# Kernel tuning notes

Hardware: AMD Instinct MI355X
Metric: run time of the kernel (lower is better)

Reference implementation:

```python
import jax, jax.numpy as jnp
import numpy as np

B, T, L = 512, 1024, 48


def setup_inputs() -> dict:
    key = jax.random.key(0)
    k1, k2, k3 = jax.random.split(key, 3)
    # one-hot gold labels [B, T, L]
    labels = jax.random.randint(k1, (B, T), 0, L)
    y_true = jax.nn.one_hot(labels, L, dtype=jnp.float32)
    y_pred = jax.random.normal(k2, (B, T, L), dtype=jnp.float32)
    trans = jax.random.normal(k3, (L, L), dtype=jnp.float32) * 0.1  # crf_trans weight
    return {"y_true": y_true, "y_pred": y_pred, "trans": trans}


def reference(y_true, y_pred, trans):
    # --- log normalization constant via forward algorithm (scan over time) ---
    init = y_pred[:, 0]                       # [B, L] initial alpha
    xs = jnp.moveaxis(y_pred[:, 1:], 1, 0)    # [T-1, B, L] emissions per step

    def step(alpha, emit):
        # alpha[b, i] + trans[i, j] -> logsumexp over i -> add emission j
        nxt = jax.nn.logsumexp(alpha[:, :, None] + trans[None, :, :], axis=1) + emit
        return nxt, None

    alpha_last, _ = jax.lax.scan(step, init, xs)          # [B, L]
    log_norm = jax.nn.logsumexp(alpha_last, axis=1, keepdims=True)  # [B, 1]

    # --- unnormalized path score: emissions + transitions along gold path ---
    point_score = jnp.sum(y_pred * y_true, axis=(1, 2))[:, None]  # [B, 1]
    trans_score = jnp.einsum("btl,lm,btm->b", y_true[:, :-1], trans, y_true[:, 1:])[:, None]

    return log_norm - point_score - trans_score  # [B, 1] negative log-likelihood
```

## Files before the change

### kernel.cpp

```cpp
#include <hip/hip_runtime.h>


constexpr int Bb = 512;
constexpr int Tt = 1024;
constexpr int Ll = 48;
constexpr int PF = 4;

#define LOG2E_F 1.44269504088896340736f
#define LN2_F   0.69314718055994530942f

__device__ __forceinline__ float rl_f(float v, int l) {
    return __uint_as_float(__builtin_amdgcn_readlane(__float_as_uint(v), (unsigned)l));
}
__device__ __forceinline__ float fexp2(float x) {
    return __builtin_amdgcn_exp2f(x);
}
__device__ __forceinline__ float flog2(float x) {
    return __builtin_amdgcn_logf(x);
}

__global__ __launch_bounds__(64)
__attribute__((amdgpu_waves_per_eu(1, 1)))
void crf_fwd_kernel(const float* __restrict__ y_true,
                    const float* __restrict__ y_pred,
                    const float* __restrict__ trans,
                    float* __restrict__ out)
{
    const int lane = threadIdx.x;

    __shared__ float str[Ll * Ll];

    if (blockIdx.x >= Bb) {
        const int b = blockIdx.x - Bb;
        for (int i = lane; i < Ll * Ll; i += 64) str[i] = trans[i];
        __syncthreads();

        const float* __restrict__ yprow = y_pred + (size_t)b * Tt * Ll;
        const float* __restrict__ ytrow = y_true + (size_t)b * Tt * Ll;

        float ps = 0.f, ts = 0.f;
        int labLast = 0;

        for (int t0 = 0; t0 < Tt; t0 += 64) {
            const int t = t0 + lane;
            const float4* row = (const float4*)(ytrow + (size_t)t * Ll);
            int lab = 0;
            #pragma unroll
            for (int k = 0; k < 12; ++k) {
                float4 v = row[k];
                if (v.x > 0.5f) lab = 4 * k + 0;
                if (v.y > 0.5f) lab = 4 * k + 1;
                if (v.z > 0.5f) lab = 4 * k + 2;
                if (v.w > 0.5f) lab = 4 * k + 3;
            }
            ps += yprow[(size_t)t * Ll + lab];
            int labPrev = __shfl_up(lab, 1);
            if (lane == 0) labPrev = labLast;
            if (t > 0) ts += str[labPrev * Ll + lab];
            labLast = __builtin_amdgcn_readlane(lab, 63);
        }

        float acc = ps + ts;
        #pragma unroll
        for (int off = 32; off >= 1; off >>= 1) acc += __shfl_xor(acc, off);
        if (lane == 0) atomicAdd(&out[b], -acc);
        return;
    }

    const int b  = blockIdx.x;
    const int ml = lane < Ll ? lane : (Ll - 1);
    const bool act = lane < Ll;
    for (int i = lane; i < Ll * Ll; i += 64) str[i] = trans[i];
    __syncthreads();

#define MK_E(l) float E##l = fexp2(str[(l) * Ll + ml] * LOG2E_F);
    MK_E(0)  MK_E(1)  MK_E(2)  MK_E(3)  MK_E(4)  MK_E(5)  MK_E(6)  MK_E(7)
    MK_E(8)  MK_E(9)  MK_E(10) MK_E(11) MK_E(12) MK_E(13) MK_E(14) MK_E(15)
    MK_E(16) MK_E(17) MK_E(18) MK_E(19) MK_E(20) MK_E(21) MK_E(22) MK_E(23)
    MK_E(24) MK_E(25) MK_E(26) MK_E(27) MK_E(28) MK_E(29) MK_E(30) MK_E(31)
    MK_E(32) MK_E(33) MK_E(34) MK_E(35) MK_E(36) MK_E(37) MK_E(38) MK_E(39)
    MK_E(40) MK_E(41) MK_E(42) MK_E(43) MK_E(44) MK_E(45) MK_E(46) MK_E(47)
#undef MK_E

    const float* __restrict__ yprow = y_pred + (size_t)b * Tt * Ll;

    float raw0 = yprow[ml];
    float e = fexp2(raw0 * LOG2E_F);
    float S = 0.f;
    float cUse = 0.5f * rl_f(raw0, 0) * LOG2E_F;

#define RLF(l, acc) acc = fmaf(rl_f(e, l), E##l, acc);

#define STEP(raw)                                                        \
    do {                                                                 \
        float cNew = 0.5f * flog2(rl_f(e, 0));                           \
        cNew = fminf(50.f, fmaxf(-50.f, cNew));                          \
        float w = fexp2(fmaf((raw), LOG2E_F, -cUse));                    \
        S += cUse;                                                       \
        cUse = cNew;                                                     \
        float a0 = 0.f, a1 = 0.f, a2 = 0.f, a3 = 0.f;                    \
        float a4 = 0.f, a5 = 0.f, a6 = 0.f, a7 = 0.f;                    \
        RLF(0,  a0) RLF(1,  a1) RLF(2,  a2) RLF(3,  a3)                  \
        RLF(4,  a4) RLF(5,  a5) RLF(6,  a6) RLF(7,  a7)                  \
        RLF(8,  a0) RLF(9,  a1) RLF(10, a2) RLF(11, a3)                  \
        RLF(12, a4) RLF(13, a5) RLF(14, a6) RLF(15, a7)                  \
        RLF(16, a0) RLF(17, a1) RLF(18, a2) RLF(19, a3)                  \
        RLF(20, a4) RLF(21, a5) RLF(22, a6) RLF(23, a7)                  \
        RLF(24, a0) RLF(25, a1) RLF(26, a2) RLF(27, a3)                  \
        RLF(28, a4) RLF(29, a5) RLF(30, a6) RLF(31, a7)                  \
        RLF(32, a0) RLF(33, a1) RLF(34, a2) RLF(35, a3)                  \
        RLF(36, a4) RLF(37, a5) RLF(38, a6) RLF(39, a7)                  \
        RLF(40, a0) RLF(41, a1) RLF(42, a2) RLF(43, a3)                  \
        RLF(44, a4) RLF(45, a5) RLF(46, a6) RLF(47, a7)                  \
        e = (((a0 + a1) + (a2 + a3)) + ((a4 + a5) + (a6 + a7))) * w;     \
    } while (0)

    float pfP[PF];
    #pragma unroll
    for (int j = 0; j < PF; ++j) pfP[j] = yprow[(1 + j) * Ll + ml];

    for (int t0 = 1; t0 <= Tt - PF - 3; t0 += PF) {
        #pragma unroll
        for (int j = 0; j < PF; ++j) {
            float raw = pfP[j];
            int tn = t0 + j + PF;
            tn = tn < Tt ? tn : (Tt - 1);
            pfP[j] = yprow[tn * Ll + ml];
            STEP(raw);
        }
    }
    STEP(pfP[0]);
    STEP(pfP[1]);
    STEP(pfP[2]);
#undef STEP
#undef RLF

    float es = act ? e : 0.f;
    #pragma unroll
    for (int off = 32; off >= 1; off >>= 1) es += __shfl_xor(es, off);

    if (lane == 0)
        atomicAdd(&out[b], LN2_F * (S + flog2(es)));
}

extern "C" void kernel_launch(void* const* d_in, const int* in_sizes, int n_in,
                              void* d_out, int out_size, void* d_ws, size_t ws_size,
                              hipStream_t stream) {
    const float* y_true = (const float*)d_in[0];
    const float* y_pred = (const float*)d_in[1];
    const float* trans  = (const float*)d_in[2];
    float* out = (float*)d_out;

    hipMemsetAsync(d_out, 0, (size_t)out_size * sizeof(float), stream);
    crf_fwd_kernel<<<2 * Bb, 64, 0, stream>>>(y_true, y_pred, trans, out);
}
```

Before: 182.8 us.

## Replace readlane broadcast matvec with DPP row_ror fmac and bpermute row rotation

The per-step 48x48 matvec previously broadcast each alpha lane with v_readlane (SALU-to-VALU round trips) before every fma. It now splits the 48 states into three 16-lane rows, fetches the two other rows with ds_bpermute, and uses v_fmac with DPP row_ror modifiers so each fma reads a rotated neighbour lane directly. The transition exponentials are precomputed in the matching rotated order using a probe of the row_ror lane mapping. This cuts the scalar readlane traffic in exchange for two LDS permutes per step and hand-written inline asm with s_nop hazard padding, which risks subtle correctness issues (lanes 48-63 use the clamped row).

```diff
diff --git a/kernel.cpp b/kernel.cpp
--- a/kernel.cpp
+++ b/kernel.cpp
@@ -12,12 +12,8 @@
 __device__ __forceinline__ float rl_f(float v, int l) {
     return __uint_as_float(__builtin_amdgcn_readlane(__float_as_uint(v), (unsigned)l));
 }
-__device__ __forceinline__ float fexp2(float x) {
-    return __builtin_amdgcn_exp2f(x);
-}
-__device__ __forceinline__ float flog2(float x) {
-    return __builtin_amdgcn_logf(x);
-}
+__device__ __forceinline__ float fexp2(float x) { return __builtin_amdgcn_exp2f(x); }
+__device__ __forceinline__ float flog2(float x) { return __builtin_amdgcn_logf(x); }
 
 __global__ __launch_bounds__(64)
 __attribute__((amdgpu_waves_per_eu(1, 1)))
@@ -70,17 +66,29 @@
     const int b  = blockIdx.x;
     const int ml = lane < Ll ? lane : (Ll - 1);
     const bool act = lane < Ll;
+    const int g = lane >> 4;
+    const int r = lane & 15;
     for (int i = lane; i < Ll * Ll; i += 64) str[i] = trans[i];
     __syncthreads();
 
-#define MK_E(l) float E##l = fexp2(str[(l) * Ll + ml] * LOG2E_F);
-    MK_E(0)  MK_E(1)  MK_E(2)  MK_E(3)  MK_E(4)  MK_E(5)  MK_E(6)  MK_E(7)
-    MK_E(8)  MK_E(9)  MK_E(10) MK_E(11) MK_E(12) MK_E(13) MK_E(14) MK_E(15)
-    MK_E(16) MK_E(17) MK_E(18) MK_E(19) MK_E(20) MK_E(21) MK_E(22) MK_E(23)
-    MK_E(24) MK_E(25) MK_E(26) MK_E(27) MK_E(28) MK_E(29) MK_E(30) MK_E(31)
-    MK_E(32) MK_E(33) MK_E(34) MK_E(35) MK_E(36) MK_E(37) MK_E(38) MK_E(39)
-    MK_E(40) MK_E(41) MK_E(42) MK_E(43) MK_E(44) MK_E(45) MK_E(46) MK_E(47)
-#undef MK_E
+#define PROBE(i) int P##i; \
+    asm volatile("s_nop 1\n\tv_mov_b32 %0, %1 row_ror:" #i : "=v"(P##i) : "v"(lane));
+    PROBE(1)  PROBE(2)  PROBE(3)  PROBE(4)  PROBE(5)  PROBE(6)  PROBE(7)
+    PROBE(8)  PROBE(9)  PROBE(10) PROBE(11) PROBE(12) PROBE(13) PROBE(14) PROBE(15)
+#undef PROBE
+
+#define MK_C(c, i, SR) float C_##c##_##i = \
+    fexp2(str[(16 * ((g + (c)) % 3) + (SR)) * Ll + ml] * LOG2E_F);
+#define MK_CI(i) MK_C(0, i, (P##i & 15)) MK_C(1, i, (P##i & 15)) MK_C(2, i, (P##i & 15))
+    MK_C(0, 0, r) MK_C(1, 0, r) MK_C(2, 0, r)
+    MK_CI(1)  MK_CI(2)  MK_CI(3)  MK_CI(4)  MK_CI(5)
+    MK_CI(6)  MK_CI(7)  MK_CI(8)  MK_CI(9)  MK_CI(10)
+    MK_CI(11) MK_CI(12) MK_CI(13) MK_CI(14) MK_CI(15)
+#undef MK_CI
+#undef MK_C
+
+    int idx1 = 4 * (16 * ((g + 1) % 3) + r);
+    int idx2 = 4 * (16 * ((g + 2) % 3) + r);
 
     const float* __restrict__ yprow = y_pred + (size_t)b * Tt * Ll;
 
@@ -89,10 +97,17 @@
     float S = 0.f;
     float cUse = 0.5f * rl_f(raw0, 0) * LOG2E_F;
 
-#define RLF(l, acc) acc = fmaf(rl_f(e, l), E##l, acc);
+#define FD(c, i, acc) asm volatile("v_fmac_f32 %0, %1, %2 row_ror:" #i \
+        : "+v"(acc) : "v"(ec##c), "v"(C_##c##_##i));
+#define F0(c, acc) asm volatile("v_fmac_f32 %0, %1, %2" \
+        : "+v"(acc) : "v"(ec##c), "v"(C_##c##_0));
 
 #define STEP(raw)                                                        \
     do {                                                                 \
+        int ei = __float_as_uint(e);                                     \
+        float ec0 = e;                                                   \
+        float ec1 = __uint_as_float((unsigned)__builtin_amdgcn_ds_bpermute(idx1, ei)); \
+        float ec2 = __uint_as_float((unsigned)__builtin_amdgcn_ds_bpermute(idx2, ei)); \
         float cNew = 0.5f * flog2(rl_f(e, 0));                           \
         cNew = fminf(50.f, fmaxf(-50.f, cNew));                          \
         float w = fexp2(fmaf((raw), LOG2E_F, -cUse));                    \
@@ -100,18 +115,19 @@
         cUse = cNew;                                                     \
         float a0 = 0.f, a1 = 0.f, a2 = 0.f, a3 = 0.f;                    \
         float a4 = 0.f, a5 = 0.f, a6 = 0.f, a7 = 0.f;                    \
-        RLF(0,  a0) RLF(1,  a1) RLF(2,  a2) RLF(3,  a3)                  \
-        RLF(4,  a4) RLF(5,  a5) RLF(6,  a6) RLF(7,  a7)                  \
-        RLF(8,  a0) RLF(9,  a1) RLF(10, a2) RLF(11, a3)                  \
-        RLF(12, a4) RLF(13, a5) RLF(14, a6) RLF(15, a7)                  \
-        RLF(16, a0) RLF(17, a1) RLF(18, a2) RLF(19, a3)                  \
-        RLF(20, a4) RLF(21, a5) RLF(22, a6) RLF(23, a7)                  \
-        RLF(24, a0) RLF(25, a1) RLF(26, a2) RLF(27, a3)                  \
-        RLF(28, a4) RLF(29, a5) RLF(30, a6) RLF(31, a7)                  \
-        RLF(32, a0) RLF(33, a1) RLF(34, a2) RLF(35, a3)                  \
-        RLF(36, a4) RLF(37, a5) RLF(38, a6) RLF(39, a7)                  \
-        RLF(40, a0) RLF(41, a1) RLF(42, a2) RLF(43, a3)                  \
-        RLF(44, a4) RLF(45, a5) RLF(46, a6) RLF(47, a7)                  \
+        asm volatile("s_nop 1");                                         \
+        F0(0, a0)      FD(0, 1,  a1) FD(0, 2,  a2) FD(0, 3,  a3)         \
+        FD(0, 4,  a4)  FD(0, 5,  a5) FD(0, 6,  a6) FD(0, 7,  a7)         \
+        FD(0, 8,  a0)  FD(0, 9,  a1) FD(0, 10, a2) FD(0, 11, a3)         \
+        FD(0, 12, a4)  FD(0, 13, a5) FD(0, 14, a6) FD(0, 15, a7)         \
+        F0(1, a0)      FD(1, 1,  a1) FD(1, 2,  a2) FD(1, 3,  a3)         \
+        FD(1, 4,  a4)  FD(1, 5,  a5) FD(1, 6,  a6) FD(1, 7,  a7)         \
+        FD(1, 8,  a0)  FD(1, 9,  a1) FD(1, 10, a2) FD(1, 11, a3)         \
+        FD(1, 12, a4)  FD(1, 13, a5) FD(1, 14, a6) FD(1, 15, a7)         \
+        F0(2, a0)      FD(2, 1,  a1) FD(2, 2,  a2) FD(2, 3,  a3)         \
+        FD(2, 4,  a4)  FD(2, 5,  a5) FD(2, 6,  a6) FD(2, 7,  a7)         \
+        FD(2, 8,  a0)  FD(2, 9,  a1) FD(2, 10, a2) FD(2, 11, a3)         \
+        FD(2, 12, a4)  FD(2, 13, a5) FD(2, 14, a6) FD(2, 15, a7)         \
         e = (((a0 + a1) + (a2 + a3)) + ((a4 + a5) + (a6 + a7))) * w;     \
     } while (0)
 
@@ -133,7 +149,8 @@
     STEP(pfP[1]);
     STEP(pfP[2]);
 #undef STEP
-#undef RLF
+#undef FD
+#undef F0
 
     float es = act ? e : 0.f;
     #pragma unroll
```

Measured after the change: 235.4 us. 28.8% more time.

## Batch 16 sequences per wave and compute CRF forward step with bf16 MFMA

Applied to the files above, without the earlier changes.

Replaces the per-sequence readlane/FMA matrix-vector product with a batched matrix product. Each wave now handles 16 sequences, and the exp(trans) times alpha step for all of them runs on bf16 MFMA 16x16x32 instructions. This cuts the forward-pass block count from 512 to 32 and removes the 48 serial readlanes per step. In exchange, alpha is rounded to bf16 at every step, which costs accuracy, and far fewer waves remain to hide the serial latency chain.

```diff
diff --git a/kernel.cpp b/kernel.cpp
--- a/kernel.cpp
+++ b/kernel.cpp
@@ -4,19 +4,27 @@
 constexpr int Bb = 512;
 constexpr int Tt = 1024;
 constexpr int Ll = 48;
-constexpr int PF = 4;
+constexpr int NC = 16;
+constexpr int NSB = Bb / NC;
 
 #define LOG2E_F 1.44269504088896340736f
 #define LN2_F   0.69314718055994530942f
 
-__device__ __forceinline__ float rl_f(float v, int l) {
-    return __uint_as_float(__builtin_amdgcn_readlane(__float_as_uint(v), (unsigned)l));
+typedef short bf16x8 __attribute__((ext_vector_type(8)));
+typedef float f32x4  __attribute__((ext_vector_type(4)));
+typedef unsigned int u32x4 __attribute__((ext_vector_type(4)));
+
+__device__ __forceinline__ float fexp2(float x) { return __builtin_amdgcn_exp2f(x); }
+__device__ __forceinline__ float flog2(float x) { return __builtin_amdgcn_logf(x); }
+
+__device__ __forceinline__ unsigned f2bf(float f) {
+    unsigned x = __float_as_uint(f);
+    return (x + 0x7FFFu + ((x >> 16) & 1u)) >> 16;
 }
-__device__ __forceinline__ float fexp2(float x) {
-    return __builtin_amdgcn_exp2f(x);
-}
-__device__ __forceinline__ float flog2(float x) {
-    return __builtin_amdgcn_logf(x);
+__device__ __forceinline__ unsigned pkbf(float lo, float hi) {
+    unsigned r;
+    asm("v_cvt_pk_bf16_f32 %0, %1, %2" : "=v"(r) : "v"(lo), "v"(hi));
+    return r;
 }
 
 __global__ __launch_bounds__(64)
@@ -27,11 +35,10 @@
                     float* __restrict__ out)
 {
     const int lane = threadIdx.x;
-
     __shared__ float str[Ll * Ll];
 
-    if (blockIdx.x >= Bb) {
-        const int b = blockIdx.x - Bb;
+    if (blockIdx.x >= NSB) {
+        const int b = blockIdx.x - NSB;
         for (int i = lane; i < Ll * Ll; i += 64) str[i] = trans[i];
         __syncthreads();
 
@@ -67,80 +74,114 @@
         return;
     }
 
-    const int b  = blockIdx.x;
-    const int ml = lane < Ll ? lane : (Ll - 1);
-    const bool act = lane < Ll;
+    const int q  = lane >> 4;
+    const int c  = lane & 15;
+    const int c4 = 4 * c;
     for (int i = lane; i < Ll * Ll; i += 64) str[i] = trans[i];
     __syncthreads();
 
-#define MK_E(l) float E##l = fexp2(str[(l) * Ll + ml] * LOG2E_F);
-    MK_E(0)  MK_E(1)  MK_E(2)  MK_E(3)  MK_E(4)  MK_E(5)  MK_E(6)  MK_E(7)
-    MK_E(8)  MK_E(9)  MK_E(10) MK_E(11) MK_E(12) MK_E(13) MK_E(14) MK_E(15)
-    MK_E(16) MK_E(17) MK_E(18) MK_E(19) MK_E(20) MK_E(21) MK_E(22) MK_E(23)
-    MK_E(24) MK_E(25) MK_E(26) MK_E(27) MK_E(28) MK_E(29) MK_E(30) MK_E(31)
-    MK_E(32) MK_E(33) MK_E(34) MK_E(35) MK_E(36) MK_E(37) MK_E(38) MK_E(39)
-    MK_E(40) MK_E(41) MK_E(42) MK_E(43) MK_E(44) MK_E(45) MK_E(46) MK_E(47)
-#undef MK_E
+    const int r0 = 4 * q;
+#define EV(r, beta) fexp2(str[(r) * Ll + 16 * (beta) + c] * LOG2E_F)
+#define MKA(beta)                                                              \
+    bf16x8 A1_##beta, A2_##beta;                                               \
+    { unsigned p0 = f2bf(EV(r0 + 0, beta)) | (f2bf(EV(r0 + 1, beta)) << 16);   \
+      unsigned p1 = f2bf(EV(r0 + 2, beta)) | (f2bf(EV(r0 + 3, beta)) << 16);   \
+      unsigned p2 = f2bf(EV(16 + r0 + 0, beta)) | (f2bf(EV(16 + r0 + 1, beta)) << 16); \
+      unsigned p3 = f2bf(EV(16 + r0 + 2, beta)) | (f2bf(EV(16 + r0 + 3, beta)) << 16); \
+      unsigned p4 = f2bf(EV(32 + r0 + 0, beta)) | (f2bf(EV(32 + r0 + 1, beta)) << 16); \
+      unsigned p5 = f2bf(EV(32 + r0 + 2, beta)) | (f2bf(EV(32 + r0 + 3, beta)) << 16); \
+      u32x4 ta = {p0, p1, p2, p3}; A1_##beta = __builtin_bit_cast(bf16x8, ta); \
+      u32x4 tb = {p4, p5, 0u, 0u}; A2_##beta = __builtin_bit_cast(bf16x8, tb); }
+    MKA(0) MKA(1) MKA(2)
+#undef MKA
+#undef EV
 
-    const float* __restrict__ yprow = y_pred + (size_t)b * Tt * Ll;
+    const float* __restrict__ ypc = y_pred + (size_t)(NC * blockIdx.x + c) * Tt * Ll;
 
-    float raw0 = yprow[ml];
-    float e = fexp2(raw0 * LOG2E_F);
+    const float4* pr0 = (const float4*)ypc;
+    float4 rv0 = pr0[q], rv1 = pr0[4 + q], rv2 = pr0[8 + q];
+    float eu00 = fexp2(rv0.x * LOG2E_F), eu01 = fexp2(rv0.y * LOG2E_F);
+    float eu02 = fexp2(rv0.z * LOG2E_F), eu03 = fexp2(rv0.w * LOG2E_F);
+    float eu10 = fexp2(rv1.x * LOG2E_F), eu11 = fexp2(rv1.y * LOG2E_F);
+    float eu12 = fexp2(rv1.z * LOG2E_F), eu13 = fexp2(rv1.w * LOG2E_F);
+    float eu20 = fexp2(rv2.x * LOG2E_F), eu21 = fexp2(rv2.y * LOG2E_F);
+    float eu22 = fexp2(rv2.z * LOG2E_F), eu23 = fexp2(rv2.w * LOG2E_F);
     float S = 0.f;
-    float cUse = 0.5f * rl_f(raw0, 0) * LOG2E_F;
+    float cUse = 0.5f * LOG2E_F * __uint_as_float(
+        (unsigned)__builtin_amdgcn_ds_bpermute(c4, __float_as_uint(rv0.x)));
 
-#define RLF(l, acc) acc = fmaf(rl_f(e, l), E##l, acc);
+    float4 pf0a, pf0b, pf0c, pf1a, pf1b, pf1c, pf2a, pf2b, pf2c, pf3a, pf3b, pf3c;
+#define LOADPF(J, tn) { const float4* pp = (const float4*)(ypc + (size_t)(tn) * Ll); \
+        pf##J##a = pp[q]; pf##J##b = pp[4 + q]; pf##J##c = pp[8 + q]; }
+    LOADPF(0, 1) LOADPF(1, 2) LOADPF(2, 3) LOADPF(3, 4)
 
-#define STEP(raw)                                                        \
-    do {                                                                 \
-        float cNew = 0.5f * flog2(rl_f(e, 0));                           \
-        cNew = fminf(50.f, fmaxf(-50.f, cNew));                          \
-        float w = fexp2(fmaf((raw), LOG2E_F, -cUse));                    \
-        S += cUse;                                                       \
-        cUse = cNew;                                                     \
-        float a0 = 0.f, a1 = 0.f, a2 = 0.f, a3 = 0.f;                    \
-        float a4 = 0.f, a5 = 0.f, a6 = 0.f, a7 = 0.f;                    \
-        RLF(0,  a0) RLF(1,  a1) RLF(2,  a2) RLF(3,  a3)                  \
-        RLF(4,  a4) RLF(5,  a5) RLF(6,  a6) RLF(7,  a7)                  \
-        RLF(8,  a0) RLF(9,  a1) RLF(10, a2) RLF(11, a3)                  \
-        RLF(12, a4) RLF(13, a5) RLF(14, a6) RLF(15, a7)                  \
-        RLF(16, a0) RLF(17, a1) RLF(18, a2) RLF(19, a3)                  \
-        RLF(20, a4) RLF(21, a5) RLF(22, a6) RLF(23, a7)                  \
-        RLF(24, a0) RLF(25, a1) RLF(26, a2) RLF(27, a3)                  \
-        RLF(28, a4) RLF(29, a5) RLF(30, a6) RLF(31, a7)                  \
-        RLF(32, a0) RLF(33, a1) RLF(34, a2) RLF(35, a3)                  \
-        RLF(36, a4) RLF(37, a5) RLF(38, a6) RLF(39, a7)                  \
-        RLF(40, a0) RLF(41, a1) RLF(42, a2) RLF(43, a3)                  \
-        RLF(44, a4) RLF(45, a5) RLF(46, a6) RLF(47, a7)                  \
-        e = (((a0 + a1) + (a2 + a3)) + ((a4 + a5) + (a6 + a7))) * w;     \
+#define STEP(J, tn)                                                            \
+    do {                                                                       \
+                            \
+        unsigned b0 = pkbf(eu00, eu01), b1 = pkbf(eu02, eu03);                 \
+        unsigned b2 = pkbf(eu10, eu11), b3 = pkbf(eu12, eu13);                 \
+        unsigned b4 = pkbf(eu20, eu21), b5 = pkbf(eu22, eu23);                 \
+        u32x4 bu1 = {b0, b1, b2, b3}; u32x4 bu2 = {b4, b5, 0u, 0u};            \
+        bf16x8 Bf1 = __builtin_bit_cast(bf16x8, bu1);                          \
+        bf16x8 Bf2 = __builtin_bit_cast(bf16x8, bu2);                          \
+                   \
+        int bp = __builtin_amdgcn_ds_bpermute(c4, __float_as_uint(eu00));      \
+                          \
+        float u00 = fexp2(fmaf(pf##J##a.x, LOG2E_F, -cUse));                   \
+        float u01 = fexp2(fmaf(pf##J##a.y, LOG2E_F, -cUse));                   \
+        float u02 = fexp2(fmaf(pf##J##a.z, LOG2E_F, -cUse));                   \
+        float u03 = fexp2(fmaf(pf##J##a.w, LOG2E_F, -cUse));                   \
+        float u10 = fexp2(fmaf(pf##J##b.x, LOG2E_F, -cUse));                   \
+        float u11 = fexp2(fmaf(pf##J##b.y, LOG2E_F, -cUse));                   \
+        float u12 = fexp2(fmaf(pf##J##b.z, LOG2E_F, -cUse));                   \
+        float u13 = fexp2(fmaf(pf##J##b.w, LOG2E_F, -cUse));                   \
+        float u20 = fexp2(fmaf(pf##J##c.x, LOG2E_F, -cUse));                   \
+        float u21 = fexp2(fmaf(pf##J##c.y, LOG2E_F, -cUse));                   \
+        float u22 = fexp2(fmaf(pf##J##c.z, LOG2E_F, -cUse));                   \
+        float u23 = fexp2(fmaf(pf##J##c.w, LOG2E_F, -cUse));                   \
+        float cNew = 0.5f * flog2(__uint_as_float((unsigned)bp));              \
+        cNew = fminf(50.f, fmaxf(-50.f, cNew));                                \
+                     \
+        f32x4 zz = {0.f, 0.f, 0.f, 0.f};                                       \
+        f32x4 d0 = __builtin_amdgcn_mfma_f32_16x16x32_bf16(A1_0, Bf1, zz, 0, 0, 0); \
+        d0 = __builtin_amdgcn_mfma_f32_16x16x32_bf16(A2_0, Bf2, d0, 0, 0, 0);  \
+        f32x4 d1 = __builtin_amdgcn_mfma_f32_16x16x32_bf16(A1_1, Bf1, zz, 0, 0, 0); \
+        d1 = __builtin_amdgcn_mfma_f32_16x16x32_bf16(A2_1, Bf2, d1, 0, 0, 0);  \
+        f32x4 d2 = __builtin_amdgcn_mfma_f32_16x16x32_bf16(A1_2, Bf1, zz, 0, 0, 0); \
+        d2 = __builtin_amdgcn_mfma_f32_16x16x32_bf16(A2_2, Bf2, d2, 0, 0, 0);  \
+                                                   \
+        LOADPF(J, tn)                                                          \
+                                                 \
+        eu00 = d0[0] * u00; eu01 = d0[1] * u01;                                \
+        eu02 = d0[2] * u02; eu03 = d0[3] * u03;                                \
+        eu10 = d1[0] * u10; eu11 = d1[1] * u11;                                \
+        eu12 = d1[2] * u12; eu13 = d1[3] * u13;                                \
+        eu20 = d2[0] * u20; eu21 = d2[1] * u21;                                \
+        eu22 = d2[2] * u22; eu23 = d2[3] * u23;                                \
+        S += cUse; cUse = cNew;                                                \
     } while (0)
 
-    float pfP[PF];
-    #pragma unroll
-    for (int j = 0; j < PF; ++j) pfP[j] = yprow[(1 + j) * Ll + ml];
+    for (int t0 = 1; t0 <= Tt - 4 - 3; t0 += 4) {
+        int tn3 = t0 + 7; tn3 = tn3 < Tt ? tn3 : (Tt - 1);
+        STEP(0, t0 + 4);
+        STEP(1, t0 + 5);
+        STEP(2, t0 + 6);
+        STEP(3, tn3);
+    }
+    STEP(0, Tt - 1);
+    STEP(1, Tt - 1);
+    STEP(2, Tt - 1);
+#undef STEP
+#undef LOADPF
 
-    for (int t0 = 1; t0 <= Tt - PF - 3; t0 += PF) {
-        #pragma unroll
-        for (int j = 0; j < PF; ++j) {
-            float raw = pfP[j];
-            int tn = t0 + j + PF;
-            tn = tn < Tt ? tn : (Tt - 1);
-            pfP[j] = yprow[tn * Ll + ml];
-            STEP(raw);
-        }
-    }
-    STEP(pfP[0]);
-    STEP(pfP[1]);
-    STEP(pfP[2]);
-#undef STEP
-#undef RLF
+    float sum = ((eu00 + eu01) + (eu02 + eu03))
+              + ((eu10 + eu11) + (eu12 + eu13))
+              + ((eu20 + eu21) + (eu22 + eu23));
+    sum += __shfl_xor(sum, 16);
+    sum += __shfl_xor(sum, 32);
 
-    float es = act ? e : 0.f;
-    #pragma unroll
-    for (int off = 32; off >= 1; off >>= 1) es += __shfl_xor(es, off);
-
-    if (lane == 0)
-        atomicAdd(&out[b], LN2_F * (S + flog2(es)));
+    float res = LN2_F * (S + flog2(sum));
+    if (lane < NC) atomicAdd(&out[NC * blockIdx.x + lane], res);
 }
 
 extern "C" void kernel_launch(void* const* d_in, const int* in_sizes, int n_in,
@@ -152,5 +193,5 @@
     float* out = (float*)d_out;
 
     hipMemsetAsync(d_out, 0, (size_t)out_size * sizeof(float), stream);
-    crf_fwd_kernel<<<2 * Bb, 64, 0, stream>>>(y_true, y_pred, trans, out);
+    crf_fwd_kernel<<<NSB + Bb, 64, 0, stream>>>(y_true, y_pred, trans, out);
 }
```

Result: slower. 255.2 us (+39.6%).

## Batch 16 sequences per wave with bf16 MFMA forward recursion over transposed emissions

Applied to the files above, without the earlier changes.

Replaces the per-sequence readlane/FMA recurrence with a 16-sequence-per-wave formulation. Each step's 48x48 exp-space matvec becomes six bf16 16x16x32 MFMAs, using a layout that interleaves emissions of 16 batch rows. Helper blocks in the same launch transpose y_pred into the workspace and signal per-tile flags, and the recurrence waves spin on those flags so the transpose overlaps the scan. The point/transition score blocks use 4 waves, and the old kernel remains as a fallback when the workspace is too small. This trades precision (bf16 inputs to the MFMA) and adds inter-block flag synchronization, which could deadlock if the consumer blocks get scheduled ahead of the producer blocks.

```diff
diff --git a/kernel.cpp b/kernel.cpp
--- a/kernel.cpp
+++ b/kernel.cpp
@@ -1,46 +1,273 @@
 #include <hip/hip_runtime.h>
 
 
-constexpr int Bb = 512;
-constexpr int Tt = 1024;
-constexpr int Ll = 48;
-constexpr int PF = 4;
+constexpr int Bb = 512, Tt = 1024, Ll = 48;
+constexpr int NC = 16, NSB = Bb / NC;
+constexpr int ROWB = NC * Ll * 4;
+constexpr size_t GRPB = (size_t)Tt * ROWB;
+constexpr size_t YPT_BYTES = (size_t)NSB * GRPB;
+constexpr int NTILE = 16;
+constexpr int NFLAG = NSB * NTILE;
 
 #define LOG2E_F 1.44269504088896340736f
 #define LN2_F   0.69314718055994530942f
 
+typedef short bf16x8 __attribute__((ext_vector_type(8)));
+typedef float f32x4  __attribute__((ext_vector_type(4)));
+typedef unsigned int u32x4 __attribute__((ext_vector_type(4)));
+
+__device__ __forceinline__ float fexp2(float x) { return __builtin_amdgcn_exp2f(x); }
+__device__ __forceinline__ float flog2(float x) { return __builtin_amdgcn_logf(x); }
 __device__ __forceinline__ float rl_f(float v, int l) {
     return __uint_as_float(__builtin_amdgcn_readlane(__float_as_uint(v), (unsigned)l));
 }
-__device__ __forceinline__ float fexp2(float x) {
-    return __builtin_amdgcn_exp2f(x);
-}
-__device__ __forceinline__ float flog2(float x) {
-    return __builtin_amdgcn_logf(x);
+__device__ __forceinline__ unsigned f2bf(float f) {
+    unsigned x = __float_as_uint(f);
+    return (x + 0x7FFFu + ((x >> 16) & 1u)) >> 16;
+}
+__device__ __forceinline__ unsigned pkbf(float lo, float hi) {
+    unsigned r;
+    asm("v_cvt_pk_bf16_f32 %0, %1, %2" : "=v"(r) : "v"(lo), "v"(hi));
+    return r;
+}
+__device__ __forceinline__ void waitflag(const unsigned* f) {
+    while (__hip_atomic_load(f, __ATOMIC_ACQUIRE, __HIP_MEMORY_SCOPE_AGENT) == 0u) {
+        __builtin_amdgcn_s_sleep(8);
+    }
+}
+
+__global__ __launch_bounds__(256)
+__attribute__((amdgpu_waves_per_eu(1, 2)))
+void crf_fwd_main(const float* __restrict__ y_true,
+                  const float* __restrict__ y_pred,
+                  const float* __restrict__ trans,
+                  float* __restrict__ out,
+                  char* __restrict__ wsb)
+{
+    const int tid = threadIdx.x;
+    unsigned* flags = (unsigned*)(wsb + YPT_BYTES);
+
+    if (blockIdx.x >= NSB && blockIdx.x < NSB + 512) {
+        const int tb = blockIdx.x - NSB;
+        const int g = tb >> 4, j = tb & 15;
+        if (tid < 192) {
+            const int c = tid / 12, k = tid % 12;
+            const float4* src = (const float4*)(y_pred + (size_t)(NC * g + c) * Tt * Ll);
+            float4* dst = (float4*)(wsb + (size_t)g * GRPB);
+            #pragma unroll 4
+            for (int r = 0; r < 64; ++r) {
+                const int t = 64 * j + r;
+                dst[(size_t)t * 192 + c * 12 + k] = src[(size_t)t * 12 + k];
+            }
+        }
+        __syncthreads();
+        if (tid == 0) {
+            __threadfence();
+            __hip_atomic_store(&flags[g * 16 + j], 1u,
+                               __ATOMIC_RELEASE, __HIP_MEMORY_SCOPE_AGENT);
+        }
+        return;
+    }
+
+    __shared__ float str[Ll * Ll];
+    __shared__ float spart[4];
+
+    if (blockIdx.x >= NSB + 512) {
+        const int b = blockIdx.x - NSB - 512;
+        for (int i = tid; i < Ll * Ll; i += 256) str[i] = trans[i];
+        __syncthreads();
+
+        const int wv = tid >> 6, lane = tid & 63;
+        const float* __restrict__ yprow = y_pred + (size_t)b * Tt * Ll;
+        const float* __restrict__ ytrow = y_true + (size_t)b * Tt * Ll;
+
+        float ps = 0.f, ts = 0.f;
+        int labLast = 0;
+        if (wv > 0) {
+            const float4* r5 = (const float4*)(ytrow + (size_t)(256 * wv - 1) * Ll);
+            int lab = 0;
+            #pragma unroll
+            for (int k = 0; k < 12; ++k) {
+                float4 v = r5[k];
+                if (v.x > 0.5f) lab = 4 * k + 0;
+                if (v.y > 0.5f) lab = 4 * k + 1;
+                if (v.z > 0.5f) lab = 4 * k + 2;
+                if (v.w > 0.5f) lab = 4 * k + 3;
+            }
+            labLast = lab;
+        }
+        for (int k = 0; k < 4; ++k) {
+            const int t = 256 * wv + 64 * k + lane;
+            const float4* row = (const float4*)(ytrow + (size_t)t * Ll);
+            int lab = 0;
+            #pragma unroll
+            for (int kk = 0; kk < 12; ++kk) {
+                float4 v = row[kk];
+                if (v.x > 0.5f) lab = 4 * kk + 0;
+                if (v.y > 0.5f) lab = 4 * kk + 1;
+                if (v.z > 0.5f) lab = 4 * kk + 2;
+                if (v.w > 0.5f) lab = 4 * kk + 3;
+            }
+            ps += yprow[(size_t)t * Ll + lab];
+            int labPrev = __shfl_up(lab, 1);
+            if (lane == 0) labPrev = labLast;
+            if (t > 0) ts += str[labPrev * Ll + lab];
+            labLast = __builtin_amdgcn_readlane(lab, 63);
+        }
+        float acc = ps + ts;
+        #pragma unroll
+        for (int off = 32; off >= 1; off >>= 1) acc += __shfl_xor(acc, off);
+        if (lane == 0) spart[wv] = acc;
+        __syncthreads();
+        if (tid == 0)
+            atomicAdd(&out[b], -((spart[0] + spart[1]) + (spart[2] + spart[3])));
+        return;
+    }
+
+    const int g = blockIdx.x;
+    for (int i = tid; i < Ll * Ll; i += 256) str[i] = trans[i];
+    __syncthreads();
+    if (tid >= 64) return;
+
+    const int lane = tid;
+    const int q = lane >> 4, c = lane & 15;
+    const int c4 = 4 * c;
+
+    const int r0 = 4 * q;
+#define EV(r, beta) fexp2(str[(r) * Ll + 16 * (beta) + c] * LOG2E_F)
+#define MKA(beta)                                                              \
+    bf16x8 A1_##beta, A2_##beta;                                               \
+    { unsigned p0 = f2bf(EV(r0 + 0, beta)) | (f2bf(EV(r0 + 1, beta)) << 16);   \
+      unsigned p1 = f2bf(EV(r0 + 2, beta)) | (f2bf(EV(r0 + 3, beta)) << 16);   \
+      unsigned p2 = f2bf(EV(16 + r0 + 0, beta)) | (f2bf(EV(16 + r0 + 1, beta)) << 16); \
+      unsigned p3 = f2bf(EV(16 + r0 + 2, beta)) | (f2bf(EV(16 + r0 + 3, beta)) << 16); \
+      unsigned p4 = f2bf(EV(32 + r0 + 0, beta)) | (f2bf(EV(32 + r0 + 1, beta)) << 16); \
+      unsigned p5 = f2bf(EV(32 + r0 + 2, beta)) | (f2bf(EV(32 + r0 + 3, beta)) << 16); \
+      u32x4 ta = {p0, p1, p2, p3}; A1_##beta = __builtin_bit_cast(bf16x8, ta); \
+      u32x4 tb = {p4, p5, 0u, 0u}; A2_##beta = __builtin_bit_cast(bf16x8, tb); }
+    MKA(0) MKA(1) MKA(2)
+#undef MKA
+#undef EV
+
+    const char* pT = wsb + (size_t)g * GRPB + (size_t)(c * 12 + q) * 16;
+    const unsigned* gflag = &flags[g * 16];
+
+    waitflag(&gflag[0]);
+    waitflag(&gflag[1]);
+    int lastW = 1;
+
+    float4 rv0 = *(const float4*)pT;
+    float4 rv1 = *(const float4*)(pT + 64);
+    float4 rv2 = *(const float4*)(pT + 128);
+    float eu00 = fexp2(rv0.x * LOG2E_F), eu01 = fexp2(rv0.y * LOG2E_F);
+    float eu02 = fexp2(rv0.z * LOG2E_F), eu03 = fexp2(rv0.w * LOG2E_F);
+    float eu10 = fexp2(rv1.x * LOG2E_F), eu11 = fexp2(rv1.y * LOG2E_F);
+    float eu12 = fexp2(rv1.z * LOG2E_F), eu13 = fexp2(rv1.w * LOG2E_F);
+    float eu20 = fexp2(rv2.x * LOG2E_F), eu21 = fexp2(rv2.y * LOG2E_F);
+    float eu22 = fexp2(rv2.z * LOG2E_F), eu23 = fexp2(rv2.w * LOG2E_F);
+    float S = 0.f;
+    float cUse = 0.5f * LOG2E_F * __uint_as_float(
+        (unsigned)__builtin_amdgcn_ds_bpermute(c4, __float_as_uint(rv0.x)));
+
+    float4 s0a, s0b, s0c, s1a, s1b, s1c, s2a, s2b, s2c, s3a, s3b, s3c,
+           s4a, s4b, s4c, s5a, s5b, s5c, s6a, s6b, s6c, s7a, s7b, s7c;
+#define REFILL(J, tn) { const char* rp_ = pT + (size_t)(tn) * ROWB;            \
+        s##J##a = *(const float4*)rp_;                                         \
+        s##J##b = *(const float4*)(rp_ + 64);                                  \
+        s##J##c = *(const float4*)(rp_ + 128); }
+    REFILL(0, 1) REFILL(1, 2) REFILL(2, 3) REFILL(3, 4)
+    REFILL(4, 5) REFILL(5, 6) REFILL(6, 7) REFILL(7, 8)
+
+#define STEP_CORE(ra, rb, rc)                                                  \
+    do {                                                                       \
+        unsigned xb0 = pkbf(eu00, eu01), xb1 = pkbf(eu02, eu03);               \
+        unsigned xb2 = pkbf(eu10, eu11), xb3 = pkbf(eu12, eu13);               \
+        unsigned xb4 = pkbf(eu20, eu21), xb5 = pkbf(eu22, eu23);               \
+        u32x4 ub1 = {xb0, xb1, xb2, xb3}; u32x4 ub2 = {xb4, xb5, 0u, 0u};      \
+        bf16x8 Bf1 = __builtin_bit_cast(bf16x8, ub1);                          \
+        bf16x8 Bf2 = __builtin_bit_cast(bf16x8, ub2);                          \
+        int bp = __builtin_amdgcn_ds_bpermute(c4, __float_as_uint(eu00));      \
+        float u00 = fexp2(fmaf((ra).x, LOG2E_F, -cUse));                       \
+        float u01 = fexp2(fmaf((ra).y, LOG2E_F, -cUse));                       \
+        float u02 = fexp2(fmaf((ra).z, LOG2E_F, -cUse));                       \
+        float u03 = fexp2(fmaf((ra).w, LOG2E_F, -cUse));                       \
+        float u10 = fexp2(fmaf((rb).x, LOG2E_F, -cUse));                       \
+        float u11 = fexp2(fmaf((rb).y, LOG2E_F, -cUse));                       \
+        float u12 = fexp2(fmaf((rb).z, LOG2E_F, -cUse));                       \
+        float u13 = fexp2(fmaf((rb).w, LOG2E_F, -cUse));                       \
+        float u20 = fexp2(fmaf((rc).x, LOG2E_F, -cUse));                       \
+        float u21 = fexp2(fmaf((rc).y, LOG2E_F, -cUse));                       \
+        float u22 = fexp2(fmaf((rc).z, LOG2E_F, -cUse));                       \
+        float u23 = fexp2(fmaf((rc).w, LOG2E_F, -cUse));                       \
+        float cNew = 0.5f * flog2(__uint_as_float((unsigned)bp));              \
+        cNew = fminf(50.f, fmaxf(-50.f, cNew));                                \
+        f32x4 zz = {0.f, 0.f, 0.f, 0.f};                                       \
+        f32x4 d0 = __builtin_amdgcn_mfma_f32_16x16x32_bf16(A1_0, Bf1, zz, 0, 0, 0); \
+        f32x4 g0 = __builtin_amdgcn_mfma_f32_16x16x32_bf16(A2_0, Bf2, zz, 0, 0, 0); \
+        f32x4 d1 = __builtin_amdgcn_mfma_f32_16x16x32_bf16(A1_1, Bf1, zz, 0, 0, 0); \
+        f32x4 g1 = __builtin_amdgcn_mfma_f32_16x16x32_bf16(A2_1, Bf2, zz, 0, 0, 0); \
+        f32x4 d2 = __builtin_amdgcn_mfma_f32_16x16x32_bf16(A1_2, Bf1, zz, 0, 0, 0); \
+        f32x4 g2 = __builtin_amdgcn_mfma_f32_16x16x32_bf16(A2_2, Bf2, zz, 0, 0, 0); \
+        d0 += g0; d1 += g1; d2 += g2;                                          \
+        eu00 = d0[0] * u00; eu01 = d0[1] * u01;                                \
+        eu02 = d0[2] * u02; eu03 = d0[3] * u03;                                \
+        eu10 = d1[0] * u10; eu11 = d1[1] * u11;                                \
+        eu12 = d1[2] * u12; eu13 = d1[3] * u13;                                \
+        eu20 = d2[0] * u20; eu21 = d2[1] * u21;                                \
+        eu22 = d2[2] * u22; eu23 = d2[3] * u23;                                \
+        S += cUse; cUse = cNew;                                                \
+    } while (0)
+
+#define STEPR(J, t0)                                                           \
+    { STEP_CORE(s##J##a, s##J##b, s##J##c);                                    \
+      int tn_ = (t0) + 8 + (J); if (tn_ > Tt - 1) tn_ = Tt - 1;                \
+      REFILL(J, tn_) }
+
+    for (int t0 = 1; t0 <= 1009; t0 += 8) {
+        int need = (t0 + 15) >> 6; if (need > 15) need = 15;
+        while (lastW < need) { ++lastW; waitflag(&gflag[lastW]); }
+        STEPR(0, t0) STEPR(1, t0) STEPR(2, t0) STEPR(3, t0)
+        STEPR(4, t0) STEPR(5, t0) STEPR(6, t0) STEPR(7, t0)
+    }
+    STEP_CORE(s0a, s0b, s0c);
+    STEP_CORE(s1a, s1b, s1c);
+    STEP_CORE(s2a, s2b, s2c);
+    STEP_CORE(s3a, s3b, s3c);
+    STEP_CORE(s4a, s4b, s4c);
+    STEP_CORE(s5a, s5b, s5c);
+    STEP_CORE(s6a, s6b, s6c);
+#undef STEPR
+#undef STEP_CORE
+#undef REFILL
+
+    float sum = ((eu00 + eu01) + (eu02 + eu03))
+              + ((eu10 + eu11) + (eu12 + eu13))
+              + ((eu20 + eu21) + (eu22 + eu23));
+    sum += __shfl_xor(sum, 16);
+    sum += __shfl_xor(sum, 32);
+
+    float res = LN2_F * (S + flog2(sum));
+    if (lane < NC) atomicAdd(&out[NC * g + lane], res);
 }
 
 __global__ __launch_bounds__(64)
 __attribute__((amdgpu_waves_per_eu(1, 1)))
-void crf_fwd_kernel(const float* __restrict__ y_true,
-                    const float* __restrict__ y_pred,
-                    const float* __restrict__ trans,
-                    float* __restrict__ out)
+void crf_fwd_small(const float* __restrict__ y_true,
+                   const float* __restrict__ y_pred,
+                   const float* __restrict__ trans,
+                   float* __restrict__ out)
 {
     const int lane = threadIdx.x;
-
     __shared__ float str[Ll * Ll];
 
     if (blockIdx.x >= Bb) {
         const int b = blockIdx.x - Bb;
         for (int i = lane; i < Ll * Ll; i += 64) str[i] = trans[i];
         __syncthreads();
-
         const float* __restrict__ yprow = y_pred + (size_t)b * Tt * Ll;
         const float* __restrict__ ytrow = y_true + (size_t)b * Tt * Ll;
-
         float ps = 0.f, ts = 0.f;
         int labLast = 0;
-
         for (int t0 = 0; t0 < Tt; t0 += 64) {
             const int t = t0 + lane;
             const float4* row = (const float4*)(ytrow + (size_t)t * Ll);
@@ -59,7 +286,6 @@
             if (t > 0) ts += str[labPrev * Ll + lab];
             labLast = __builtin_amdgcn_readlane(lab, 63);
         }
-
         float acc = ps + ts;
         #pragma unroll
         for (int off = 32; off >= 1; off >>= 1) acc += __shfl_xor(acc, off);
@@ -67,12 +293,11 @@
         return;
     }
 
-    const int b  = blockIdx.x;
+    const int b = blockIdx.x;
     const int ml = lane < Ll ? lane : (Ll - 1);
     const bool act = lane < Ll;
     for (int i = lane; i < Ll * Ll; i += 64) str[i] = trans[i];
     __syncthreads();
-
 #define MK_E(l) float E##l = fexp2(str[(l) * Ll + ml] * LOG2E_F);
     MK_E(0)  MK_E(1)  MK_E(2)  MK_E(3)  MK_E(4)  MK_E(5)  MK_E(6)  MK_E(7)
     MK_E(8)  MK_E(9)  MK_E(10) MK_E(11) MK_E(12) MK_E(13) MK_E(14) MK_E(15)
@@ -81,17 +306,13 @@
     MK_E(32) MK_E(33) MK_E(34) MK_E(35) MK_E(36) MK_E(37) MK_E(38) MK_E(39)
     MK_E(40) MK_E(41) MK_E(42) MK_E(43) MK_E(44) MK_E(45) MK_E(46) MK_E(47)
 #undef MK_E
-
     const float* __restrict__ yprow = y_pred + (size_t)b * Tt * Ll;
-
     float raw0 = yprow[ml];
     float e = fexp2(raw0 * LOG2E_F);
     float S = 0.f;
     float cUse = 0.5f * rl_f(raw0, 0) * LOG2E_F;
-
 #define RLF(l, acc) acc = fmaf(rl_f(e, l), E##l, acc);
-
-#define STEP(raw)                                                        \
+#define FSTEP(raw)                                                       \
     do {                                                                 \
         float cNew = 0.5f * flog2(rl_f(e, 0));                           \
         cNew = fminf(50.f, fmaxf(-50.f, cNew));                          \
@@ -114,33 +335,26 @@
         RLF(44, a4) RLF(45, a5) RLF(46, a6) RLF(47, a7)                  \
         e = (((a0 + a1) + (a2 + a3)) + ((a4 + a5) + (a6 + a7))) * w;     \
     } while (0)
-
-    float pfP[PF];
+    float pfP[4];
     #pragma unroll
-    for (int j = 0; j < PF; ++j) pfP[j] = yprow[(1 + j) * Ll + ml];
-
-    for (int t0 = 1; t0 <= Tt - PF - 3; t0 += PF) {
+    for (int j = 0; j < 4; ++j) pfP[j] = yprow[(1 + j) * Ll + ml];
+    for (int t0 = 1; t0 <= Tt - 7; t0 += 4) {
         #pragma unroll
-        for (int j = 0; j < PF; ++j) {
+        for (int j = 0; j < 4; ++j) {
             float raw = pfP[j];
-            int tn = t0 + j + PF;
+            int tn = t0 + j + 4;
             tn = tn < Tt ? tn : (Tt - 1);
             pfP[j] = yprow[tn * Ll + ml];
-            STEP(raw);
-        }
-    }
-    STEP(pfP[0]);
-    STEP(pfP[1]);
-    STEP(pfP[2]);
-#undef STEP
+            FSTEP(raw);
+        }
+    }
+    FSTEP(pfP[0]); FSTEP(pfP[1]); FSTEP(pfP[2]);
+#undef FSTEP
 #undef RLF
-
     float es = act ? e : 0.f;
     #pragma unroll
     for (int off = 32; off >= 1; off >>= 1) es += __shfl_xor(es, off);
-
-    if (lane == 0)
-        atomicAdd(&out[b], LN2_F * (S + flog2(es)));
+    if (lane == 0) atomicAdd(&out[b], LN2_F * (S + flog2(es)));
 }
 
 extern "C" void kernel_launch(void* const* d_in, const int* in_sizes, int n_in,
@@ -152,5 +366,12 @@
     float* out = (float*)d_out;
 
     hipMemsetAsync(d_out, 0, (size_t)out_size * sizeof(float), stream);
-    crf_fwd_kernel<<<2 * Bb, 64, 0, stream>>>(y_true, y_pred, trans, out);
-}
+    const size_t need = YPT_BYTES + (size_t)NFLAG * sizeof(unsigned);
+    if (ws_size >= need) {
+        hipMemsetAsync((char*)d_ws + YPT_BYTES, 0, NFLAG * sizeof(unsigned), stream);
+        crf_fwd_main<<<NSB + 512 + Bb, 256, 0, stream>>>(
+            y_true, y_pred, trans, out, (char*)d_ws);
+    } else {
+        crf_fwd_small<<<2 * Bb, 64, 0, stream>>>(y_true, y_pred, trans, out);
+    }
+}
```

Measured after the change: 524.6 us. +187.0%, slower.
